# Optimization experiments

Hardware: AMD Instinct MI355X
Metric: run time of the kernel (lower is better)

The kernel has to match this reference:

```python
import math
import jax, jax.numpy as jnp
import numpy as np

INF = 10000000000.0
B, S, D = 4, 4096, 64


def setup_inputs() -> dict:
    key = jax.random.key(0)
    kq, kk, kv = jax.random.split(key, 3)
    query = jax.random.normal(kq, (B, S, D), dtype=jnp.float32)
    k = jax.random.normal(kk, (B, S, D), dtype=jnp.float32)
    value = jax.random.normal(kv, (B, S, D), dtype=jnp.float32)
    padding = jnp.zeros((B, S), dtype=bool)  # True = masked-out key position
    return {"query": query, "key": k, "value": value, "padding": padding}


def reference(query, key, value, padding):
    # Faithful to torch Attention.forward with causal=True, dropout=0.
    scale = math.sqrt(query.shape[-1])  # sqrt(d_key)
    # [B, Sq, Sk] scores
    dot = jnp.einsum("bqd,bkd->bqk", query, key)
    Sk = key.shape[1]
    # causal: subtract INF on strict upper triangle (applied BEFORE scaling, as in source)
    tri = jnp.triu(jnp.ones((Sk, Sk), dtype=dot.dtype), 1) * INF
    dot = dot - tri[None, :, :]
    # padding mask: set masked key columns to -INF
    dot = jnp.where(padding[:, None, :], -INF, dot)
    probs = jax.nn.softmax(dot / scale, axis=-1)
    return jnp.einsum("bqk,bkd->bqd", probs, value)
```

## Files before the change

kernel.cpp:

```cpp
#include <hip/hip_runtime.h>
#include <hip/hip_bf16.h>


#define S_LEN 4096
#define D_DIM 64
#define NBATCH 4
#define QBLK 128
#define KVBLK 64
#define NQB (S_LEN / QBLK)
#define SLOT_B 17408

typedef __attribute__((ext_vector_type(16))) float f32x16;
typedef __attribute__((ext_vector_type(4))) float f32x4;
typedef __attribute__((ext_vector_type(8))) short s16x8;
typedef __attribute__((ext_vector_type(4))) short s16x4;
typedef __attribute__((ext_vector_type(2))) unsigned int u32x2;

#define FK(n) ((((n) ^ ((n) >> 3)) & 7) << 4)
#define FV(d) (((((d) & 7) << 4)) ^ ((((d) >> 3) & 1) << 3))

__device__ __forceinline__ unsigned short f2bfu(float f) {
  return __builtin_bit_cast(unsigned short, __float2bfloat16(f));
}
__device__ __forceinline__ unsigned pk2(float a, float b) {
  return (unsigned)f2bfu(a) | ((unsigned)f2bfu(b) << 16);
}
__device__ __forceinline__ float bf2f(short s) {
  return __builtin_bit_cast(float, ((unsigned)(unsigned short)s) << 16);
}

__global__ __launch_bounds__(256, 3) void fattn_partial(
    const float* __restrict__ Qg, const float* __restrict__ Kg,
    const float* __restrict__ Vg, const unsigned char* __restrict__ Pad,
    char* __restrict__ Ws, int CL, int TOTC)
{
  const int wid = blockIdx.x;
  const int b   = wid & 3;
  const int u   = TOTC - 1 - (wid >> 2);
  int Qb = 0, ci = 0;
  {
    int uu = u, q = 0;
    while (true) {
      const int nch = (2 * q + 2 + CL - 1) / CL;
      if (uu < nch) { ci = uu; break; }
      uu -= nch; ++q;
    }
    Qb = q;
  }
  const int q0  = Qb * QBLK;
  const int ntt = 2 * Qb + 2;
  const int t0  = ci * CL;
  const int t1  = (t0 + CL < ntt) ? (t0 + CL) : ntt;

  const int tid = threadIdx.x;
  const int w   = tid >> 6;
  const int l   = tid & 63;
  const int ql  = l & 31;
  const int hi  = l >> 5;
  const int qw0 = q0 + 32 * w;
  const int qa  = qw0 + ql;

  const int sq  = l & 3;
  const int sm  = (l >> 2) & 3;
  const int sc2 = l >> 4;
  const int snb = 4 * w + 16 * sc2;

  __shared__ short Ksh[2][KVBLK * D_DIM];
  __shared__ short Vtsh[2][D_DIM * KVBLK];
  __shared__ int anyPadSh;

  const unsigned char* PadB = Pad + (size_t)b * S_LEN;

  if (tid == 0) anyPadSh = 0;
  __syncthreads();
  {
    const int nk  = (t1 - t0) * KVBLK;
    const int idx = 2 * tid;
    if (idx < nk) {
      const unsigned char* pp = PadB + t0 * KVBLK + idx;
      const bool nz = pp[0] || ((idx + 1 < nk) ? pp[1] : (unsigned char)0);
      if (nz) anyPadSh = 1;
    }
  }

  s16x8 qf[4];
  {
    const float* qp = Qg + ((size_t)(b * S_LEN + qa)) * D_DIM + 8 * hi;
    #pragma unroll
    for (int dc = 0; dc < 4; ++dc)
      #pragma unroll
      for (int j = 0; j < 8; ++j)
        qf[dc][j] = (short)f2bfu(qp[16 * dc + j] * 0.125f);
  }

  f32x16 acc[2];
  #pragma unroll
  for (int dt = 0; dt < 2; ++dt)
    #pragma unroll
    for (int i = 0; i < 16; ++i) acc[dt][i] = 0.f;
  float mrow = -INFINITY;
  float lrow = 0.f;

  u32x2 kpb[4], vpb[4];

#define LOAD_K(T) do {                                                       \
    const int kv0_ = (T) * KVBLK;                                            \
    _Pragma("unroll")                                                        \
    for (int s_ = 0; s_ < 4; ++s_) {                                         \
      const size_t go_ =                                                     \
          ((size_t)(b * S_LEN + kv0_ + snb + sq)) * D_DIM + 16 * s_ + 4 * sm;\
      const float4 kx = *(const float4*)(Kg + go_);                          \
      kpb[s_][0] = pk2(kx.x, kx.y); kpb[s_][1] = pk2(kx.z, kx.w);            \
    }                                                                        \
  } while (0)

#define LOAD_V(T) do {                                                       \
    const int kv0_ = (T) * KVBLK;                                            \
    _Pragma("unroll")                                                        \
    for (int s_ = 0; s_ < 4; ++s_) {                                         \
      const size_t go_ =                                                     \
          ((size_t)(b * S_LEN + kv0_ + snb + sq)) * D_DIM + 16 * s_ + 4 * sm;\
      const float4 vx = *(const float4*)(Vg + go_);                          \
      vpb[s_][0] = pk2(vx.x, vx.y); vpb[s_][1] = pk2(vx.z, vx.w);            \
    }                                                                        \
  } while (0)

#define STAGE(BUF) do {                                                      \
    _Pragma("unroll")                                                        \
    for (int s_ = 0; s_ < 4; ++s_) {                                         \
      const int d0_ = 16 * s_ + 4 * sm; const int nk_ = snb + sq;            \
      *(u32x2*)((char*)&Ksh[BUF][0] + nk_ * 128 + ((2 * d0_) ^ FK(nk_))) =   \
          kpb[s_];                                                           \
      unsigned u0 = vpb[s_][0], u1 = vpb[s_][1];                             \
      unsigned x_ = (sq & 2) ? u0 : u1;                                      \
      unsigned y_ = __shfl_xor(x_, 2);                                       \
      unsigned A0 = (sq & 2) ? y_ : u0;                                      \
      unsigned A1 = (sq & 2) ? u1 : y_;                                      \
      unsigned z0 = __shfl_xor(A0, 1);                                       \
      unsigned z1 = __shfl_xor(A1, 1);                                       \
      unsigned o0, o1;                                                       \
      if (sq & 1) { o0 = (z0 >> 16) | (A0 & 0xFFFF0000u);                    \
                    o1 = (z1 >> 16) | (A1 & 0xFFFF0000u); }                  \
      else        { o0 = (A0 & 0xFFFFu) | (z0 << 16);                        \
                    o1 = (A1 & 0xFFFFu) | (z1 << 16); }                      \
      const int dv_ = d0_ + sq;                                              \
      u32x2 vv2; vv2[0] = o0; vv2[1] = o1;                                   \
      *(u32x2*)((char*)&Vtsh[BUF][0] + dv_ * 128 + ((2 * snb) ^ FV(dv_))) = vv2;\
    }                                                                        \
  } while (0)

  LOAD_K(t0);
  LOAD_V(t0);
  STAGE(0);
  __syncthreads();
  const bool hasPad = (anyPadSh != 0);
  int cb = 0;

  for (int t = t0; t < t1; ++t) {
    const int kv0 = t * KVBLK;
    const bool more = (t + 1 < t1);
    if (more) LOAD_K(t + 1);

    f32x16 sv[2];
    __builtin_amdgcn_s_setprio(1);
    #pragma unroll
    for (int kt = 0; kt < 2; ++kt) {
      f32x16 a;
      #pragma unroll
      for (int i = 0; i < 16; ++i) a[i] = 0.f;
      #pragma unroll
      for (int dc = 0; dc < 4; ++dc) {
        const int nr = 32 * kt + ql;
        const s16x8 kf = *(const s16x8*)((char*)&Ksh[cb][0] + nr * 128 +
                                         ((32 * dc + 16 * hi) ^ FK(nr)));
        a = __builtin_amdgcn_mfma_f32_32x32x16_bf16(kf, qf[dc], a, 0, 0, 0);
      }
      sv[kt] = a;
    }
    __builtin_amdgcn_s_setprio(0);

    if (more) LOAD_V(t + 1);

    if (hasPad) {
      #pragma unroll
      for (int kt = 0; kt < 2; ++kt)
        #pragma unroll
        for (int r1 = 0; r1 < 4; ++r1) {
          const unsigned pd =
              *(const unsigned*)(PadB + kv0 + 32 * kt + 8 * r1 + 4 * hi);
          #pragma unroll
          for (int r0 = 0; r0 < 4; ++r0)
            if ((pd >> (8 * r0)) & 0xFFu) sv[kt][4 * r1 + r0] = -1e30f;
        }
    }
    #pragma unroll
    for (int kt = 0; kt < 2; ++kt) {
      const int kvt = kv0 + 32 * kt;
      if (kvt + 31 > qw0) {
        #pragma unroll
        for (int r1 = 0; r1 < 4; ++r1)
          #pragma unroll
          for (int r0 = 0; r0 < 4; ++r0)
            if (kvt + 8 * r1 + 4 * hi + r0 > qa) sv[kt][4 * r1 + r0] = -1e30f;
      }
    }

    f32x16 mx;
    #pragma unroll
    for (int i = 0; i < 16; ++i) mx[i] = fmaxf(sv[0][i], sv[1][i]);
    f32x4 m4;
    #pragma unroll
    for (int i = 0; i < 4; ++i)
      m4[i] = fmaxf(fmaxf(mx[i], mx[i + 4]), fmaxf(mx[i + 8], mx[i + 12]));
    float vm = fmaxf(fmaxf(m4[0], m4[1]), fmaxf(m4[2], m4[3]));
    vm = fmaxf(vm, __shfl_xor(vm, 32));
    const float mn   = fmaxf(mrow, vm);
    const float corr = __expf(mrow - mn);
    mrow = mn;
    lrow *= corr;
    #pragma unroll
    for (int dt = 0; dt < 2; ++dt)
      #pragma unroll
      for (int i = 0; i < 16; ++i) acc[dt][i] *= corr;

    float rs0 = 0.f, rs1 = 0.f, rs2 = 0.f, rs3 = 0.f;
    #pragma unroll
    for (int kt = 0; kt < 2; ++kt)
      #pragma unroll
      for (int i4 = 0; i4 < 16; i4 += 4) {
        const float p0 = __expf(sv[kt][i4 + 0] - mn);
        const float p1 = __expf(sv[kt][i4 + 1] - mn);
        const float p2 = __expf(sv[kt][i4 + 2] - mn);
        const float p3 = __expf(sv[kt][i4 + 3] - mn);
        sv[kt][i4 + 0] = p0; sv[kt][i4 + 1] = p1;
        sv[kt][i4 + 2] = p2; sv[kt][i4 + 3] = p3;
        rs0 += p0; rs1 += p1; rs2 += p2; rs3 += p3;
      }
    lrow += (rs0 + rs1) + (rs2 + rs3);

    __builtin_amdgcn_s_setprio(1);
    #pragma unroll
    for (int sk = 0; sk < 4; ++sk) {
      const int kt = sk >> 1, rb = 8 * (sk & 1);
      union { unsigned u[4]; s16x8 v; } pb;
      pb.u[0] = pk2(sv[kt][rb + 0], sv[kt][rb + 1]);
      pb.u[1] = pk2(sv[kt][rb + 2], sv[kt][rb + 3]);
      pb.u[2] = pk2(sv[kt][rb + 4], sv[kt][rb + 5]);
      pb.u[3] = pk2(sv[kt][rb + 6], sv[kt][rb + 7]);
      #pragma unroll
      for (int dt = 0; dt < 2; ++dt) {
        const int dr = 32 * dt + ql;
        const char* vrow = (char*)&Vtsh[cb][0] + dr * 128;
        const s16x4 v0 = *(const s16x4*)(vrow + ((32 * sk + 8 * hi) ^ FV(dr)));
        const s16x4 v1 = *(const s16x4*)(vrow + ((32 * sk + 16 + 8 * hi) ^ FV(dr)));
        s16x8 vf;
        vf[0] = v0[0]; vf[1] = v0[1]; vf[2] = v0[2]; vf[3] = v0[3];
        vf[4] = v1[0]; vf[5] = v1[1]; vf[6] = v1[2]; vf[7] = v1[3];
        acc[dt] = __builtin_amdgcn_mfma_f32_32x32x16_bf16(vf, pb.v, acc[dt], 0, 0, 0);
      }
    }
    __builtin_amdgcn_s_setprio(0);

    if (more) STAGE(cb ^ 1);
    __syncthreads();
    cb ^= 1;
  }

  const float lt = lrow + __shfl_xor(lrow, 32);

  char* slot = Ws + ((size_t)b * TOTC + u) * SLOT_B;
  const int row = 32 * w + ql;
  #pragma unroll
  for (int dt = 0; dt < 2; ++dt)
    #pragma unroll
    for (int r1 = 0; r1 < 4; ++r1) {
      u32x2 p;
      p[0] = pk2(acc[dt][4 * r1 + 0], acc[dt][4 * r1 + 1]);
      p[1] = pk2(acc[dt][4 * r1 + 2], acc[dt][4 * r1 + 3]);
      *(u32x2*)(slot + row * 128 + (32 * dt + 8 * r1 + 4 * hi) * 2) = p;
    }
  if (hi == 0) {
    ((float*)(slot + 16384))[row]       = mrow;
    ((float*)(slot + 16384 + 512))[row] = lt;
  }
}

__global__ __launch_bounds__(256, 8) void fattn_merge(
    const char* __restrict__ Ws, float* __restrict__ Og, int CL, int TOTC)
{
  const int blk = blockIdx.x;
  const int qbi = blk >> 2;
  const int qr  = blk & 3;
  const int Qb  = qbi & (NQB - 1);
  const int b   = qbi >> 5;
  const int tid = threadIdx.x;
  const int row = 32 * qr + (tid >> 3);
  const int d0  = (tid & 7) * 8;

  const int ntt    = 2 * Qb + 2;
  const int nvalid = (ntt + CL - 1) / CL;
  int pre = 0;
  for (int q = 0; q < Qb; ++q) pre += (2 * q + 2 + CL - 1) / CL;

  const char* base = Ws + ((size_t)b * TOTC + pre) * SLOT_B;

  float mstar = -INFINITY;
  for (int ci = 0; ci < nvalid; ++ci)
    mstar = fmaxf(mstar, ((const float*)(base + (size_t)ci * SLOT_B + 16384))[row]);

  float lsum = 0.f;
  float o[8];
  #pragma unroll
  for (int k = 0; k < 8; ++k) o[k] = 0.f;

  for (int ci = 0; ci < nvalid; ++ci) {
    const char* slot = base + (size_t)ci * SLOT_B;
    const float wgt = __expf(((const float*)(slot + 16384))[row] - mstar);
    lsum += wgt * ((const float*)(slot + 16384 + 512))[row];
    const s16x8 ov = *(const s16x8*)(slot + row * 128 + d0 * 2);
    #pragma unroll
    for (int k = 0; k < 8; ++k) o[k] += wgt * bf2f(ov[k]);
  }

  const float inv = 1.0f / lsum;
  float* op = Og + ((size_t)(b * S_LEN + Qb * QBLK + row)) * D_DIM + d0;
  f32x4 o0, o1;
  #pragma unroll
  for (int k = 0; k < 4; ++k) { o0[k] = o[k] * inv; o1[k] = o[4 + k] * inv; }
  *(f32x4*)(op) = o0;
  *(f32x4*)(op + 4) = o1;
}

extern "C" void kernel_launch(void* const* d_in, const int* in_sizes, int n_in,
                              void* d_out, int out_size, void* d_ws, size_t ws_size,
                              hipStream_t stream) {
  const float* Q = (const float*)d_in[0];
  const float* K = (const float*)d_in[1];
  const float* V = (const float*)d_in[2];
  const unsigned char* P = (const unsigned char*)d_in[3];
  float* O  = (float*)d_out;
  char*  Ws = (char*)d_ws;

  int CL = 4;
  int TOTC = 0;
  for (int q = 0; q < NQB; ++q) TOTC += (2 * q + 2 + CL - 1) / CL;
  if (ws_size < (size_t)NBATCH * TOTC * SLOT_B) {
    CL = 8;
    TOTC = 0;
    for (int q = 0; q < NQB; ++q) TOTC += (2 * q + 2 + CL - 1) / CL;
  }

  dim3 grid(NBATCH * TOTC);
  dim3 block(256);
  hipLaunchKernelGGL(fattn_partial, grid, block, 0, stream, Q, K, V, P, Ws,
                     CL, TOTC);
  hipLaunchKernelGGL(fattn_merge, dim3(NBATCH * NQB * 4), dim3(256), 0, stream,
                     Ws, O, CL, TOTC);
}
```

Baseline: 60.09 us.

## Fuse split-KV merge into partial kernel via last-block atomic counter

Removes the separate merge kernel. Each partial block increments a per-query-block atomic counter, and the last block to finish combines all partial results and writes the output. Query blocks covered by a single chunk now write normalized output directly, skipping the workspace round trip. This adds a memset launch, threadfence and atomic overhead, plus a serialized merge tail handled by 256 threads with 32 accumulators each.

```diff
diff --git a/kernel.cpp b/kernel.cpp
--- a/kernel.cpp
+++ b/kernel.cpp
@@ -32,12 +32,13 @@
 __global__ __launch_bounds__(256, 3) void fattn_partial(
     const float* __restrict__ Qg, const float* __restrict__ Kg,
     const float* __restrict__ Vg, const unsigned char* __restrict__ Pad,
-    char* __restrict__ Ws, int CL, int TOTC)
+    float* __restrict__ Og, char* __restrict__ Ws,
+    unsigned* __restrict__ cnt, int CL, int TOTC)
 {
   const int wid = blockIdx.x;
   const int b   = wid & 3;
   const int u   = TOTC - 1 - (wid >> 2);
-  int Qb = 0, ci = 0;
+  int Qb = 0, ci = 0, pre = 0;
   {
     int uu = u, q = 0;
     while (true) {
@@ -45,12 +46,14 @@
       if (uu < nch) { ci = uu; break; }
       uu -= nch; ++q;
     }
-    Qb = q;
-  }
-  const int q0  = Qb * QBLK;
-  const int ntt = 2 * Qb + 2;
-  const int t0  = ci * CL;
-  const int t1  = (t0 + CL < ntt) ? (t0 + CL) : ntt;
+    Qb  = q;
+    pre = u - ci;
+  }
+  const int q0     = Qb * QBLK;
+  const int ntt    = 2 * Qb + 2;
+  const int nvalid = (ntt + CL - 1) / CL;
+  const int t0     = ci * CL;
+  const int t1     = (t0 + CL < ntt) ? (t0 + CL) : ntt;
 
   const int tid = threadIdx.x;
   const int w   = tid >> 6;
@@ -67,11 +70,11 @@
 
   __shared__ short Ksh[2][KVBLK * D_DIM];
   __shared__ short Vtsh[2][D_DIM * KVBLK];
-  __shared__ int anyPadSh;
+  __shared__ int flagSh;
 
   const unsigned char* PadB = Pad + (size_t)b * S_LEN;
 
-  if (tid == 0) anyPadSh = 0;
+  if (tid == 0) flagSh = 0;
   __syncthreads();
   {
     const int nk  = (t1 - t0) * KVBLK;
@@ -79,7 +82,7 @@
     if (idx < nk) {
       const unsigned char* pp = PadB + t0 * KVBLK + idx;
       const bool nz = pp[0] || ((idx + 1 < nk) ? pp[1] : (unsigned char)0);
-      if (nz) anyPadSh = 1;
+      if (nz) flagSh = 1;
     }
   }
 
@@ -153,7 +156,7 @@
   LOAD_V(t0);
   STAGE(0);
   __syncthreads();
-  const bool hasPad = (anyPadSh != 0);
+  const bool hasPad = (flagSh != 0);
   int cb = 0;
 
   for (int t = t0; t < t1; ++t) {
@@ -268,6 +271,21 @@
 
   const float lt = lrow + __shfl_xor(lrow, 32);
 
+  if (nvalid == 1) {
+    const float inv = 1.0f / lt;
+    #pragma unroll
+    for (int dt = 0; dt < 2; ++dt)
+      #pragma unroll
+      for (int r1 = 0; r1 < 4; ++r1) {
+        f32x4 o;
+        #pragma unroll
+        for (int r0 = 0; r0 < 4; ++r0) o[r0] = acc[dt][4 * r1 + r0] * inv;
+        *(f32x4*)(Og + ((size_t)(b * S_LEN + qa)) * D_DIM +
+                  32 * dt + 8 * r1 + 4 * hi) = o;
+      }
+    return;
+  }
+
   char* slot = Ws + ((size_t)b * TOTC + u) * SLOT_B;
   const int row = 32 * w + ql;
   #pragma unroll
@@ -283,52 +301,52 @@
     ((float*)(slot + 16384))[row]       = mrow;
     ((float*)(slot + 16384 + 512))[row] = lt;
   }
-}
-
-__global__ __launch_bounds__(256, 8) void fattn_merge(
-    const char* __restrict__ Ws, float* __restrict__ Og, int CL, int TOTC)
-{
-  const int blk = blockIdx.x;
-  const int qbi = blk >> 2;
-  const int qr  = blk & 3;
-  const int Qb  = qbi & (NQB - 1);
-  const int b   = qbi >> 5;
-  const int tid = threadIdx.x;
-  const int row = 32 * qr + (tid >> 3);
-  const int d0  = (tid & 7) * 8;
-
-  const int ntt    = 2 * Qb + 2;
-  const int nvalid = (ntt + CL - 1) / CL;
-  int pre = 0;
-  for (int q = 0; q < Qb; ++q) pre += (2 * q + 2 + CL - 1) / CL;
-
-  const char* base = Ws + ((size_t)b * TOTC + pre) * SLOT_B;
+
+  __syncthreads();
+  if (tid == 0) {
+    __threadfence();
+    const unsigned v = atomicAdd(&cnt[b * NQB + Qb], 1u);
+    flagSh = (v == (unsigned)(nvalid - 1)) ? 1 : 0;
+  }
+  __syncthreads();
+  if (!flagSh) return;
+  __threadfence();
+
+  const int mr = tid >> 1;
+  const int md = (tid & 1) << 5;
+  const char* mbase = Ws + ((size_t)b * TOTC + pre) * SLOT_B;
 
   float mstar = -INFINITY;
-  for (int ci = 0; ci < nvalid; ++ci)
-    mstar = fmaxf(mstar, ((const float*)(base + (size_t)ci * SLOT_B + 16384))[row]);
+  for (int c2 = 0; c2 < nvalid; ++c2)
+    mstar = fmaxf(mstar,
+                  ((const float*)(mbase + (size_t)c2 * SLOT_B + 16384))[mr]);
 
   float lsum = 0.f;
-  float o[8];
+  float o[32];
   #pragma unroll
-  for (int k = 0; k < 8; ++k) o[k] = 0.f;
-
-  for (int ci = 0; ci < nvalid; ++ci) {
-    const char* slot = base + (size_t)ci * SLOT_B;
-    const float wgt = __expf(((const float*)(slot + 16384))[row] - mstar);
-    lsum += wgt * ((const float*)(slot + 16384 + 512))[row];
-    const s16x8 ov = *(const s16x8*)(slot + row * 128 + d0 * 2);
-    #pragma unroll
-    for (int k = 0; k < 8; ++k) o[k] += wgt * bf2f(ov[k]);
+  for (int k = 0; k < 32; ++k) o[k] = 0.f;
+
+  for (int c2 = 0; c2 < nvalid; ++c2) {
+    const char* sl = mbase + (size_t)c2 * SLOT_B;
+    const float wgt = __expf(((const float*)(sl + 16384))[mr] - mstar);
+    lsum += wgt * ((const float*)(sl + 16384 + 512))[mr];
+    #pragma unroll
+    for (int g8 = 0; g8 < 4; ++g8) {
+      const s16x8 ov = *(const s16x8*)(sl + mr * 128 + (md + 8 * g8) * 2);
+      #pragma unroll
+      for (int k = 0; k < 8; ++k) o[8 * g8 + k] += wgt * bf2f(ov[k]);
+    }
   }
 
   const float inv = 1.0f / lsum;
-  float* op = Og + ((size_t)(b * S_LEN + Qb * QBLK + row)) * D_DIM + d0;
-  f32x4 o0, o1;
+  float* op = Og + ((size_t)(b * S_LEN + q0 + mr)) * D_DIM + md;
   #pragma unroll
-  for (int k = 0; k < 4; ++k) { o0[k] = o[k] * inv; o1[k] = o[4 + k] * inv; }
-  *(f32x4*)(op) = o0;
-  *(f32x4*)(op + 4) = o1;
+  for (int g4 = 0; g4 < 8; ++g4) {
+    f32x4 ov;
+    #pragma unroll
+    for (int k = 0; k < 4; ++k) ov[k] = o[4 * g4 + k] * inv;
+    *(f32x4*)(op + 4 * g4) = ov;
+  }
 }
 
 extern "C" void kernel_launch(void* const* d_in, const int* in_sizes, int n_in,
@@ -344,16 +362,17 @@
   int CL = 4;
   int TOTC = 0;
   for (int q = 0; q < NQB; ++q) TOTC += (2 * q + 2 + CL - 1) / CL;
-  if (ws_size < (size_t)NBATCH * TOTC * SLOT_B) {
+  if (ws_size < (size_t)NBATCH * TOTC * SLOT_B + 512) {
     CL = 8;
     TOTC = 0;
     for (int q = 0; q < NQB; ++q) TOTC += (2 * q + 2 + CL - 1) / CL;
   }
+  unsigned* cnt = (unsigned*)(Ws + (size_t)NBATCH * TOTC * SLOT_B);
+
+  hipMemsetAsync(cnt, 0, NBATCH * NQB * sizeof(unsigned), stream);
 
   dim3 grid(NBATCH * TOTC);
   dim3 block(256);
-  hipLaunchKernelGGL(fattn_partial, grid, block, 0, stream, Q, K, V, P, Ws,
-                     CL, TOTC);
-  hipLaunchKernelGGL(fattn_merge, dim3(NBATCH * NQB * 4), dim3(256), 0, stream,
-                     Ws, O, CL, TOTC);
-}
+  hipLaunchKernelGGL(fattn_partial, grid, block, 0, stream, Q, K, V, P, O, Ws,
+                     cnt, CL, TOTC);
+}
```

After: 131.0 us. +117.9%, slower.

## Switch K/V LDS staging from double buffer to single buffer with register prefetch

Applied to the files above, without the earlier changes.

Replaces the double-buffered K and V shared-memory tiles with a single buffer. Each iteration now stages the prefetched registers, synchronises, issues the next K and V global loads together, then computes. This halves LDS use, which may allow more resident workgroups. In exchange it adds a second barrier per iteration and serialises staging with compute. The pad flag is now read from shared memory on every iteration.

```diff
diff --git a/kernel.cpp b/kernel.cpp
--- a/kernel.cpp
+++ b/kernel.cpp
@@ -65,8 +65,8 @@
   const int sc2 = l >> 4;
   const int snb = 4 * w + 16 * sc2;
 
-  __shared__ short Ksh[2][KVBLK * D_DIM];
-  __shared__ short Vtsh[2][D_DIM * KVBLK];
+  __shared__ short Ksh[KVBLK * D_DIM];
+  __shared__ short Vtsh[D_DIM * KVBLK];
   __shared__ int anyPadSh;
 
   const unsigned char* PadB = Pad + (size_t)b * S_LEN;
@@ -103,33 +103,24 @@
 
   u32x2 kpb[4], vpb[4];
 
-#define LOAD_K(T) do {                                                       \
+#define LOAD_KV(T) do {                                                      \
     const int kv0_ = (T) * KVBLK;                                            \
     _Pragma("unroll")                                                        \
     for (int s_ = 0; s_ < 4; ++s_) {                                         \
       const size_t go_ =                                                     \
           ((size_t)(b * S_LEN + kv0_ + snb + sq)) * D_DIM + 16 * s_ + 4 * sm;\
       const float4 kx = *(const float4*)(Kg + go_);                          \
+      const float4 vx = *(const float4*)(Vg + go_);                          \
       kpb[s_][0] = pk2(kx.x, kx.y); kpb[s_][1] = pk2(kx.z, kx.w);            \
-    }                                                                        \
-  } while (0)
-
-#define LOAD_V(T) do {                                                       \
-    const int kv0_ = (T) * KVBLK;                                            \
-    _Pragma("unroll")                                                        \
-    for (int s_ = 0; s_ < 4; ++s_) {                                         \
-      const size_t go_ =                                                     \
-          ((size_t)(b * S_LEN + kv0_ + snb + sq)) * D_DIM + 16 * s_ + 4 * sm;\
-      const float4 vx = *(const float4*)(Vg + go_);                          \
       vpb[s_][0] = pk2(vx.x, vx.y); vpb[s_][1] = pk2(vx.z, vx.w);            \
     }                                                                        \
   } while (0)
 
-#define STAGE(BUF) do {                                                      \
+#define STAGE() do {                                                         \
     _Pragma("unroll")                                                        \
     for (int s_ = 0; s_ < 4; ++s_) {                                         \
       const int d0_ = 16 * s_ + 4 * sm; const int nk_ = snb + sq;            \
-      *(u32x2*)((char*)&Ksh[BUF][0] + nk_ * 128 + ((2 * d0_) ^ FK(nk_))) =   \
+      *(u32x2*)((char*)&Ksh[0] + nk_ * 128 + ((2 * d0_) ^ FK(nk_))) =        \
           kpb[s_];                                                           \
       unsigned u0 = vpb[s_][0], u1 = vpb[s_][1];                             \
       unsigned x_ = (sq & 2) ? u0 : u1;                                      \
@@ -145,21 +136,19 @@
                     o1 = (A1 & 0xFFFFu) | (z1 << 16); }                      \
       const int dv_ = d0_ + sq;                                              \
       u32x2 vv2; vv2[0] = o0; vv2[1] = o1;                                   \
-      *(u32x2*)((char*)&Vtsh[BUF][0] + dv_ * 128 + ((2 * snb) ^ FV(dv_))) = vv2;\
+      *(u32x2*)((char*)&Vtsh[0] + dv_ * 128 + ((2 * snb) ^ FV(dv_))) = vv2;  \
     }                                                                        \
   } while (0)
 
-  LOAD_K(t0);
-  LOAD_V(t0);
-  STAGE(0);
-  __syncthreads();
-  const bool hasPad = (anyPadSh != 0);
-  int cb = 0;
+  LOAD_KV(t0);
 
   for (int t = t0; t < t1; ++t) {
+    STAGE();
+    __syncthreads();
+    const bool more = (t + 1 < t1);
+    if (more) LOAD_KV(t + 1);
+
     const int kv0 = t * KVBLK;
-    const bool more = (t + 1 < t1);
-    if (more) LOAD_K(t + 1);
 
     f32x16 sv[2];
     __builtin_amdgcn_s_setprio(1);
@@ -171,7 +160,7 @@
       #pragma unroll
       for (int dc = 0; dc < 4; ++dc) {
         const int nr = 32 * kt + ql;
-        const s16x8 kf = *(const s16x8*)((char*)&Ksh[cb][0] + nr * 128 +
+        const s16x8 kf = *(const s16x8*)((char*)&Ksh[0] + nr * 128 +
                                          ((32 * dc + 16 * hi) ^ FK(nr)));
         a = __builtin_amdgcn_mfma_f32_32x32x16_bf16(kf, qf[dc], a, 0, 0, 0);
       }
@@ -179,9 +168,7 @@
     }
     __builtin_amdgcn_s_setprio(0);
 
-    if (more) LOAD_V(t + 1);
-
-    if (hasPad) {
+    if (anyPadSh) {
       #pragma unroll
       for (int kt = 0; kt < 2; ++kt)
         #pragma unroll
@@ -250,7 +237,7 @@
       #pragma unroll
       for (int dt = 0; dt < 2; ++dt) {
         const int dr = 32 * dt + ql;
-        const char* vrow = (char*)&Vtsh[cb][0] + dr * 128;
+        const char* vrow = (char*)&Vtsh[0] + dr * 128;
         const s16x4 v0 = *(const s16x4*)(vrow + ((32 * sk + 8 * hi) ^ FV(dr)));
         const s16x4 v1 = *(const s16x4*)(vrow + ((32 * sk + 16 + 8 * hi) ^ FV(dr)));
         s16x8 vf;
@@ -261,9 +248,7 @@
     }
     __builtin_amdgcn_s_setprio(0);
 
-    if (more) STAGE(cb ^ 1);
     __syncthreads();
-    cb ^= 1;
   }
 
   const float lt = lrow + __shfl_xor(lrow, 32);
```

After: 59.04 us. Within noise of the previous version (-1.7%).
